# Optimization experiments

Hardware: AMD Instinct MI355X
Metric: run time of the kernel (lower is better)

The kernel has to match this reference:

```python
import jax, jax.numpy as jnp
import numpy as np

TAU = 0.1
LAMBD = 0.75
EPS = 1e-8  # torch cosine_similarity norm clamp


def setup_inputs() -> dict:
    key = jax.random.key(0)
    k1, k2 = jax.random.split(key)
    B, D = 8192, 768
    v = jax.random.normal(k1, (B, D), dtype=jnp.float32)
    u = jax.random.normal(k2, (B, D), dtype=jnp.float32)
    return {"v": v, "u": u}


def reference(v, u):
    # Batched equivalent of the per-sample Python loop:
    # cos(v_i, u_j) = <v_i/||v_i||, u_j/||u_j||>, with torch's eps clamp on norms.
    v = v.astype(jnp.float32)
    u = u.astype(jnp.float32)
    vn = v / jnp.maximum(jnp.linalg.norm(v, axis=1, keepdims=True), EPS)
    un = u / jnp.maximum(jnp.linalg.norm(u, axis=1, keepdims=True), EPS)
    sim = jnp.einsum('id,jd->ij', vn, un) / TAU  # [B, B] logits
    diag = jnp.diagonal(sim)
    # image->text: -log( exp(sim_ii) / sum_j exp(sim_ij) )
    loss_it = jax.nn.logsumexp(sim, axis=1) - diag
    # text->image: -log( exp(sim_ii) / sum_j exp(sim_ji) )
    loss_ti = jax.nn.logsumexp(sim, axis=0) - diag
    # In the torch source text_image calls .item(), detaching it from autograd.
    loss_ti = jax.lax.stop_gradient(loss_ti)
    return jnp.mean(LAMBD * loss_it + (1.0 - LAMBD) * loss_ti)
```

## Files before the change

### kernel.cpp

```cpp
#include <hip/hip_runtime.h>
#include <hip/hip_bf16.h>

typedef unsigned char u8;
typedef unsigned short u16;
typedef unsigned int u32;
typedef float f32x16 __attribute__((ext_vector_type(16)));
typedef float f32x2 __attribute__((ext_vector_type(2)));
typedef int i32x4 __attribute__((ext_vector_type(4)));
typedef int i32x8 __attribute__((ext_vector_type(8)));

#define B_SZ 8192
#define D_SZ 768
#define TAU_INV 10.0f
#define ESCALE 0.014088818758681283f
#define FP4_SCALE 32.0f
#define SCHRAU_K1 118185.58f
#define SCHRAU_K2 1064879685.0f


__device__ __forceinline__ u32 fp4_enc(float x) {
    float y = fabsf(x);
    u32 n = (u32)(y >= 0.25f) + (u32)(y >= 0.75f) + (u32)(y >= 1.25f) +
            (u32)(y >= 1.75f) + (u32)(y >= 2.5f)  + (u32)(y >= 3.5f) +
            (u32)(y >= 5.0f);
    return n | (x < 0.f ? 8u : 0u);
}

__device__ __forceinline__ u16 fp4_pack4(float x, float y, float z, float w) {
    return (u16)(fp4_enc(x) | (fp4_enc(y) << 4) | (fp4_enc(z) << 8) | (fp4_enc(w) << 12));
}

__global__ __launch_bounds__(256) void norm_kernel(const float4* __restrict__ v,
                                                   const float4* __restrict__ u,
                                                   u16* __restrict__ vn,
                                                   u16* __restrict__ un,
                                                   float* __restrict__ diag) {
    const int wid = threadIdx.x >> 6, lane = threadIdx.x & 63;
    const int row = blockIdx.x * 4 + wid;
    const float4* vr = v + (size_t)row * 192;
    const float4* ur = u + (size_t)row * 192;
    float4 a[3], b[3];
    float sv = 0.f, su = 0.f, sd = 0.f;
#pragma unroll
    for (int c = 0; c < 3; ++c) {
        a[c] = vr[lane + 64 * c];
        b[c] = ur[lane + 64 * c];
        sv += a[c].x * a[c].x + a[c].y * a[c].y + a[c].z * a[c].z + a[c].w * a[c].w;
        su += b[c].x * b[c].x + b[c].y * b[c].y + b[c].z * b[c].z + b[c].w * b[c].w;
        sd += a[c].x * b[c].x + a[c].y * b[c].y + a[c].z * b[c].z + a[c].w * b[c].w;
    }
#pragma unroll
    for (int m = 1; m < 64; m <<= 1) {
        sv += __shfl_xor(sv, m);
        su += __shfl_xor(su, m);
        sd += __shfl_xor(sd, m);
    }
    const float iv = FP4_SCALE / fmaxf(sqrtf(sv), 1e-8f);
    const float iu = FP4_SCALE / fmaxf(sqrtf(su), 1e-8f);
    const int rg = row >> 5, rr = row & 31;
#pragma unroll
    for (int c = 0; c < 3; ++c) {
        u16 pa = fp4_pack4(a[c].x * iv, a[c].y * iv, a[c].z * iv, a[c].w * iv);
        u16 pb = fp4_pack4(b[c].x * iu, b[c].y * iu, b[c].z * iu, b[c].w * iu);
        const int e = lane + 64 * c;
        const int idx = (rg * 12 + (e >> 4)) * 512 + ((e >> 3) & 1) * 256 + rr * 8 + (e & 7);
        vn[idx] = pa;
        un[idx] = pb;
    }
    if (lane == 0) diag[row] = sd * iv * iu * TAU_INV / (FP4_SCALE * FP4_SCALE);
}

__device__ __forceinline__ i32x8 ldsfrag(const u8* p) {
    i32x4 lo = *(const i32x4*)p;
    return __builtin_shufflevector(lo, lo, 0, 1, 2, 3, -1, -1, -1, -1);
}

__device__ __forceinline__ void gload_lds16(const u8* g, u8* l) {
    __builtin_amdgcn_global_load_lds((const __attribute__((address_space(1))) void*)g,
                                     (__attribute__((address_space(3))) void*)l, 16, 0, 0);
}

__device__ __forceinline__ f32x16 mx_mfma4(i32x8 a, i32x8 b, f32x16 c) {
    return __builtin_amdgcn_mfma_scale_f32_32x32x64_f8f6f4(
        a, b, c, 4, 4, 0, 0x7F7F7F7F, 0, 0x7F7F7F7F);
}

__global__ __launch_bounds__(1024, 4) void simexp_kernel(const u8* __restrict__ vn,
                                                         const u8* __restrict__ un,
                                                         float* __restrict__ rowP,
                                                         float* __restrict__ colP) {
    __shared__ __attribute__((aligned(16))) u8 stg[3][16][1024];
    __shared__ float rowLds[4][256];
    __shared__ float colLds[4][256];

    const int tid  = threadIdx.x;
    const int w    = tid >> 6;
    const int lane = tid & 63;
    const int l32  = lane & 31;
    const int h    = lane >> 5;
    const int wr = w >> 2, wc = w & 3;

    const int id = blockIdx.x;
    const int chunk = id >> 6;
    const int li = id & 63;
    const int rb = ((chunk >> 2) << 3) + (li >> 3);
    const int cb = ((chunk & 3) << 3) + (li & 7);

    const u8* gsrc = (w < 8 ? vn + (size_t)(rb * 8 + w) * 12288
                            : un + (size_t)(cb * 8 + (w - 8)) * 12288)
                     + (u32)lane * 16;

    f32x16 acc[2][2];
#pragma unroll
    for (int i = 0; i < 2; ++i)
#pragma unroll
        for (int j = 0; j < 2; ++j)
#pragma unroll
            for (int r = 0; r < 16; ++r) acc[i][j][r] = 0.f;

#define STAGE(t) gload_lds16(gsrc + (t) * 1024, &stg[(t) % 3][w][0]);

    STAGE(0)
    STAGE(1)
    asm volatile("s_waitcnt vmcnt(1)\n\ts_barrier" ::: "memory");

#pragma unroll
    for (int t = 0; t < 12; ++t) {
        if (t + 2 < 12) STAGE(t + 2)
        const u8* base = &stg[t % 3][0][0] + (u32)lane * 16;
        i32x8 fa0 = ldsfrag(base + (wr * 2)     * 1024);
        i32x8 fa1 = ldsfrag(base + (wr * 2 + 1) * 1024);
        i32x8 fb0 = ldsfrag(base + (8 + wc * 2) * 1024);
        i32x8 fb1 = ldsfrag(base + (9 + wc * 2) * 1024);
        __builtin_amdgcn_s_setprio(1);
        acc[0][0] = mx_mfma4(fa0, fb0, acc[0][0]);
        acc[1][0] = mx_mfma4(fa1, fb0, acc[1][0]);
        acc[0][1] = mx_mfma4(fa0, fb1, acc[0][1]);
        acc[1][1] = mx_mfma4(fa1, fb1, acc[1][1]);
        __builtin_amdgcn_s_setprio(0);
        if (t < 10)       asm volatile("s_waitcnt vmcnt(1)\n\ts_barrier" ::: "memory");
        else if (t == 10) asm volatile("s_waitcnt vmcnt(0)\n\ts_barrier" ::: "memory");
    }
#undef STAGE

    f32x2 val2[16];
    f32x2 cacc2[2];
#pragma unroll
    for (int p = 0; p < 16; ++p) { val2[p].x = 0.f; val2[p].y = 0.f; }
    cacc2[0].x = 0.f; cacc2[0].y = 0.f;
    cacc2[1].x = 0.f; cacc2[1].y = 0.f;
#pragma unroll
    for (int i = 0; i < 2; ++i)
#pragma unroll
        for (int j = 0; j < 2; ++j)
#pragma unroll
            for (int r = 0; r < 16; r += 2) {
                f32x2 a;
                a.x = acc[i][j][r];
                a.y = acc[i][j][r + 1];
                f32x2 t = a * SCHRAU_K1 + SCHRAU_K2;
                f32x2 e;
                e.x = __int_as_float((int)t.x);
                e.y = __int_as_float((int)t.y);
                val2[i * 8 + (r >> 1)] += e;
                cacc2[j] += e;
            }

#pragma unroll
    for (int m = 16; m >= 2; m >>= 1) {
        const int n = m >> 1;
        const bool hi = (l32 & m) != 0;
#pragma unroll
        for (int p = 0; p < n; ++p) {
            f32x2 a = val2[p], b = val2[p + n];
            f32x2 x, y;
            x.x = hi ? b.x : a.x;  x.y = hi ? b.y : a.y;
            y.x = hi ? a.x : b.x;  y.y = hi ? a.y : b.y;
            f32x2 s;
            s.x = __shfl_xor(y.x, m);
            s.y = __shfl_xor(y.y, m);
            val2[p] = x + s;
        }
    }
    {
        f32x2 s;
        s.x = __shfl_xor(val2[0].x, 1);
        s.y = __shfl_xor(val2[0].y, 1);
        val2[0] += s;
    }
    {
        const int q = (l32 >> 1) & 15;
        const int t = 2 * q + (l32 & 1);
        const int i = t >> 4, r = t & 15;
        const int row = wr * 64 + i * 32 + (r & 3) + 8 * (r >> 2) + 4 * h;
        rowLds[wc][row] = (l32 & 1) ? val2[0].y : val2[0].x;
    }
    {
        float c0 = cacc2[0].x + cacc2[0].y;
        float c1 = cacc2[1].x + cacc2[1].y;
        c0 += __shfl_xor(c0, 32);
        c1 += __shfl_xor(c1, 32);
        if (h == 0) {
            colLds[wr][wc * 64 + l32]      = c0;
            colLds[wr][wc * 64 + 32 + l32] = c1;
        }
    }
    __syncthreads();
    if (tid < 256) {
        rowP[(size_t)cb * B_SZ + rb * 256 + tid] =
            rowLds[0][tid] + rowLds[1][tid] + rowLds[2][tid] + rowLds[3][tid];
    } else if (tid < 512) {
        const int t = tid - 256;
        colP[(size_t)rb * B_SZ + cb * 256 + t] =
            colLds[0][t] + colLds[1][t] + colLds[2][t] + colLds[3][t];
    }
}

__global__ __launch_bounds__(256) void finalize_kernel(const float* __restrict__ rowP,
                                                       const float* __restrict__ colP,
                                                       const float* __restrict__ diag,
                                                       float* __restrict__ out) {
    const int i = blockIdx.x * 256 + threadIdx.x;
    float rs = 0.f, cs = 0.f;
#pragma unroll 8
    for (int p = 0; p < 32; ++p) {
        rs += rowP[(size_t)p * B_SZ + i];
        cs += colP[(size_t)p * B_SZ + i];
    }
    float contrib = (0.75f * logf(rs) + 0.25f * logf(cs) - diag[i]) * (1.0f / (float)B_SZ);
#pragma unroll
    for (int m = 1; m < 64; m <<= 1) contrib += __shfl_xor(contrib, m);
    __shared__ float red[4];
    const int wid = threadIdx.x >> 6, lane = threadIdx.x & 63;
    if (lane == 0) red[wid] = contrib;
    __syncthreads();
    if (threadIdx.x == 0) atomicAdd(out, red[0] + red[1] + red[2] + red[3]);
}

extern "C" void kernel_launch(void* const* d_in, const int* in_sizes, int n_in,
                              void* d_out, int out_size, void* d_ws, size_t ws_size,
                              hipStream_t stream) {
    const float* v = (const float*)d_in[0];
    const float* u = (const float*)d_in[1];
    char* ws = (char*)d_ws;
    u16* vn4   = (u16*)(ws);
    u16* un4   = (u16*)(ws + 3145728);
    float* dg  = (float*)(ws + 6291456);
    float* rwp = (float*)(ws + 6324224);
    float* clp = (float*)(ws + 7372800);
    float* out = (float*)d_out;

    hipMemsetAsync(out, 0, sizeof(float), stream);
    hipLaunchKernelGGL(norm_kernel, dim3(2048), dim3(256), 0, stream,
                       (const float4*)v, (const float4*)u, vn4, un4, dg);
    hipLaunchKernelGGL(simexp_kernel, dim3(1024), dim3(1024), 0, stream,
                       (const u8*)vn4, (const u8*)un4, rwp, clp);
    hipLaunchKernelGGL(finalize_kernel, dim3(B_SZ / 256), dim3(256), 0, stream, rwp, clp, dg, out);
}
```

Measured before the change: 125.5 us.

## Use 8-wave blocks with 128x64 per-wave tiles and double-K staging

Cuts the similarity/exp kernel from 16 waves to 8 waves per 256x256 block. Each wave now computes a 128x64 tile with 8 accumulators instead of 64x64 with 4, and each stage loads two K-chunks. This is meant to raise MFMA work per LDS fragment load, halve the number of barriers, and reduce cross-wave reductions. The cost is higher register pressure and fewer waves available to hide latency.

```diff
diff --git a/kernel.cpp b/kernel.cpp
--- a/kernel.cpp
+++ b/kernel.cpp
@@ -85,13 +85,13 @@
         a, b, c, 4, 4, 0, 0x7F7F7F7F, 0, 0x7F7F7F7F);
 }
 
-__global__ __launch_bounds__(1024, 4) void simexp_kernel(const u8* __restrict__ vn,
-                                                         const u8* __restrict__ un,
-                                                         float* __restrict__ rowP,
-                                                         float* __restrict__ colP) {
-    __shared__ __attribute__((aligned(16))) u8 stg[3][16][1024];
+__global__ __launch_bounds__(512, 2) void simexp_kernel(const u8* __restrict__ vn,
+                                                        const u8* __restrict__ un,
+                                                        float* __restrict__ rowP,
+                                                        float* __restrict__ colP) {
+    __shared__ __attribute__((aligned(16))) u8 stg[3][16][2][1024];
     __shared__ float rowLds[4][256];
-    __shared__ float colLds[4][256];
+    __shared__ float colLds[2][256];
 
     const int tid  = threadIdx.x;
     const int w    = tid >> 6;
@@ -106,51 +106,68 @@
     const int rb = ((chunk >> 2) << 3) + (li >> 3);
     const int cb = ((chunk & 3) << 3) + (li & 7);
 
-    const u8* gsrc = (w < 8 ? vn + (size_t)(rb * 8 + w) * 12288
-                            : un + (size_t)(cb * 8 + (w - 8)) * 12288)
-                     + (u32)lane * 16;
-
-    f32x16 acc[2][2];
-#pragma unroll
-    for (int i = 0; i < 2; ++i)
+    const u8* gA = vn + (size_t)(rb * 8 + w) * 12288 + (u32)lane * 16;
+    const u8* gB = un + (size_t)(cb * 8 + w) * 12288 + (u32)lane * 16;
+
+    f32x16 acc[4][2];
+#pragma unroll
+    for (int i = 0; i < 4; ++i)
 #pragma unroll
         for (int j = 0; j < 2; ++j)
 #pragma unroll
             for (int r = 0; r < 16; ++r) acc[i][j][r] = 0.f;
 
-#define STAGE(t) gload_lds16(gsrc + (t) * 1024, &stg[(t) % 3][w][0]);
+#define STAGE(t)                                                  \
+    {                                                             \
+        gload_lds16(gA + (2 * (t)) * 1024,     &stg[(t) % 3][w][0][0]);     \
+        gload_lds16(gA + (2 * (t) + 1) * 1024, &stg[(t) % 3][w][1][0]);     \
+        gload_lds16(gB + (2 * (t)) * 1024,     &stg[(t) % 3][8 + w][0][0]); \
+        gload_lds16(gB + (2 * (t) + 1) * 1024, &stg[(t) % 3][8 + w][1][0]); \
+    }
 
     STAGE(0)
     STAGE(1)
-    asm volatile("s_waitcnt vmcnt(1)\n\ts_barrier" ::: "memory");
-
-#pragma unroll
-    for (int t = 0; t < 12; ++t) {
-        if (t + 2 < 12) STAGE(t + 2)
-        const u8* base = &stg[t % 3][0][0] + (u32)lane * 16;
-        i32x8 fa0 = ldsfrag(base + (wr * 2)     * 1024);
-        i32x8 fa1 = ldsfrag(base + (wr * 2 + 1) * 1024);
-        i32x8 fb0 = ldsfrag(base + (8 + wc * 2) * 1024);
-        i32x8 fb1 = ldsfrag(base + (9 + wc * 2) * 1024);
-        __builtin_amdgcn_s_setprio(1);
-        acc[0][0] = mx_mfma4(fa0, fb0, acc[0][0]);
-        acc[1][0] = mx_mfma4(fa1, fb0, acc[1][0]);
-        acc[0][1] = mx_mfma4(fa0, fb1, acc[0][1]);
-        acc[1][1] = mx_mfma4(fa1, fb1, acc[1][1]);
-        __builtin_amdgcn_s_setprio(0);
-        if (t < 10)       asm volatile("s_waitcnt vmcnt(1)\n\ts_barrier" ::: "memory");
-        else if (t == 10) asm volatile("s_waitcnt vmcnt(0)\n\ts_barrier" ::: "memory");
+    asm volatile("s_waitcnt vmcnt(4)\n\ts_barrier" ::: "memory");
+
+#pragma unroll
+    for (int t = 0; t < 6; ++t) {
+        if (t + 2 < 6) STAGE(t + 2)
+        const u8* s = &stg[t % 3][0][0][0] + (u32)lane * 16;
+#pragma unroll
+        for (int kk = 0; kk < 2; ++kk) {
+            i32x8 fa0 = ldsfrag(s + ((wr * 4 + 0) * 2 + kk) * 1024);
+            i32x8 fa1 = ldsfrag(s + ((wr * 4 + 1) * 2 + kk) * 1024);
+            i32x8 fa2 = ldsfrag(s + ((wr * 4 + 2) * 2 + kk) * 1024);
+            i32x8 fa3 = ldsfrag(s + ((wr * 4 + 3) * 2 + kk) * 1024);
+            i32x8 fb0 = ldsfrag(s + ((8 + wc * 2 + 0) * 2 + kk) * 1024);
+            i32x8 fb1 = ldsfrag(s + ((8 + wc * 2 + 1) * 2 + kk) * 1024);
+            __builtin_amdgcn_s_setprio(1);
+            acc[0][0] = mx_mfma4(fa0, fb0, acc[0][0]);
+            acc[1][0] = mx_mfma4(fa1, fb0, acc[1][0]);
+            acc[2][0] = mx_mfma4(fa2, fb0, acc[2][0]);
+            acc[3][0] = mx_mfma4(fa3, fb0, acc[3][0]);
+            acc[0][1] = mx_mfma4(fa0, fb1, acc[0][1]);
+            acc[1][1] = mx_mfma4(fa1, fb1, acc[1][1]);
+            acc[2][1] = mx_mfma4(fa2, fb1, acc[2][1]);
+            acc[3][1] = mx_mfma4(fa3, fb1, acc[3][1]);
+            __builtin_amdgcn_s_setprio(0);
+        }
+        if (t < 4)       asm volatile("s_waitcnt vmcnt(4)\n\ts_barrier" ::: "memory");
+        else if (t == 4) asm volatile("s_waitcnt vmcnt(0)\n\ts_barrier" ::: "memory");
     }
 #undef STAGE
 
-    f32x2 val2[16];
+    f32x2 va[16], vb[16];
     f32x2 cacc2[2];
 #pragma unroll
-    for (int p = 0; p < 16; ++p) { val2[p].x = 0.f; val2[p].y = 0.f; }
+    for (int p = 0; p < 16; ++p) {
+        va[p].x = 0.f; va[p].y = 0.f;
+        vb[p].x = 0.f; vb[p].y = 0.f;
+    }
     cacc2[0].x = 0.f; cacc2[0].y = 0.f;
     cacc2[1].x = 0.f; cacc2[1].y = 0.f;
 #pragma unroll
-    for (int i = 0; i < 2; ++i)
+    for (int i = 0; i < 4; ++i)
 #pragma unroll
         for (int j = 0; j < 2; ++j)
 #pragma unroll
@@ -162,7 +179,8 @@
                 f32x2 e;
                 e.x = __int_as_float((int)t.x);
                 e.y = __int_as_float((int)t.y);
-                val2[i * 8 + (r >> 1)] += e;
+                if (i < 2) va[(i & 1) * 8 + (r >> 1)] += e;
+                else       vb[(i & 1) * 8 + (r >> 1)] += e;
                 cacc2[j] += e;
             }
 
@@ -172,28 +190,44 @@
         const bool hi = (l32 & m) != 0;
 #pragma unroll
         for (int p = 0; p < n; ++p) {
-            f32x2 a = val2[p], b = val2[p + n];
-            f32x2 x, y;
-            x.x = hi ? b.x : a.x;  x.y = hi ? b.y : a.y;
-            y.x = hi ? a.x : b.x;  y.y = hi ? a.y : b.y;
-            f32x2 s;
-            s.x = __shfl_xor(y.x, m);
-            s.y = __shfl_xor(y.y, m);
-            val2[p] = x + s;
+            {
+                f32x2 a = va[p], b = va[p + n];
+                f32x2 x, y;
+                x.x = hi ? b.x : a.x;  x.y = hi ? b.y : a.y;
+                y.x = hi ? a.x : b.x;  y.y = hi ? a.y : b.y;
+                f32x2 s;
+                s.x = __shfl_xor(y.x, m);
+                s.y = __shfl_xor(y.y, m);
+                va[p] = x + s;
+            }
+            {
+                f32x2 a = vb[p], b = vb[p + n];
+                f32x2 x, y;
+                x.x = hi ? b.x : a.x;  x.y = hi ? b.y : a.y;
+                y.x = hi ? a.x : b.x;  y.y = hi ? a.y : b.y;
+                f32x2 s;
+                s.x = __shfl_xor(y.x, m);
+                s.y = __shfl_xor(y.y, m);
+                vb[p] = x + s;
+            }
         }
     }
     {
         f32x2 s;
-        s.x = __shfl_xor(val2[0].x, 1);
-        s.y = __shfl_xor(val2[0].y, 1);
-        val2[0] += s;
+        s.x = __shfl_xor(va[0].x, 1);
+        s.y = __shfl_xor(va[0].y, 1);
+        va[0] += s;
+        s.x = __shfl_xor(vb[0].x, 1);
+        s.y = __shfl_xor(vb[0].y, 1);
+        vb[0] += s;
     }
     {
         const int q = (l32 >> 1) & 15;
-        const int t = 2 * q + (l32 & 1);
-        const int i = t >> 4, r = t & 15;
-        const int row = wr * 64 + i * 32 + (r & 3) + 8 * (r >> 2) + 4 * h;
-        rowLds[wc][row] = (l32 & 1) ? val2[0].y : val2[0].x;
+        const int tt = 2 * q + (l32 & 1);
+        const int i2 = tt >> 4, r2 = tt & 15;
+        const int rbase = i2 * 32 + (r2 & 3) + 8 * (r2 >> 2) + 4 * h;
+        rowLds[wc][wr * 128 + rbase]      = (l32 & 1) ? va[0].y : va[0].x;
+        rowLds[wc][wr * 128 + 64 + rbase] = (l32 & 1) ? vb[0].y : vb[0].x;
     }
     {
         float c0 = cacc2[0].x + cacc2[0].y;
@@ -209,10 +243,9 @@
     if (tid < 256) {
         rowP[(size_t)cb * B_SZ + rb * 256 + tid] =
             rowLds[0][tid] + rowLds[1][tid] + rowLds[2][tid] + rowLds[3][tid];
-    } else if (tid < 512) {
+    } else {
         const int t = tid - 256;
-        colP[(size_t)rb * B_SZ + cb * 256 + t] =
-            colLds[0][t] + colLds[1][t] + colLds[2][t] + colLds[3][t];
+        colP[(size_t)rb * B_SZ + cb * 256 + t] = colLds[0][t] + colLds[1][t];
     }
 }
 
@@ -253,7 +286,7 @@
     hipMemsetAsync(out, 0, sizeof(float), stream);
     hipLaunchKernelGGL(norm_kernel, dim3(2048), dim3(256), 0, stream,
                        (const float4*)v, (const float4*)u, vn4, un4, dg);
-    hipLaunchKernelGGL(simexp_kernel, dim3(1024), dim3(1024), 0, stream,
+    hipLaunchKernelGGL(simexp_kernel, dim3(1024), dim3(512), 0, stream,
                        (const u8*)vn4, (const u8*)un4, rwp, clp);
     hipLaunchKernelGGL(finalize_kernel, dim3(B_SZ / 256), dim3(256), 0, stream, rwp, clp, dg, out);
 }
```

Measured after the change: 129.2 us. +3.0%, slower.

## Retile similarity kernel to 256x128 tiles with 512-thread blocks and deeper k-steps

Applied to the files above, without the earlier changes.

Blocks go from 1024 threads computing 256x256 tiles to 512 threads (8 waves) computing 256x128 tiles. Each pipeline stage now loads 2 KB k-slices, so there are 6 stages of two MFMA k-steps each, and every wave issues three LDS-direct loads per stage. Block IDs are remapped for L2 locality, and the reduction scratch reuses the staging LDS. The finalize kernel now sums 64 row partials instead of 32. Smaller blocks may schedule more flexibly, but the smaller column tile costs reuse of the v operand and doubles the row-partial traffic.

```diff
diff --git a/kernel.cpp b/kernel.cpp
--- a/kernel.cpp
+++ b/kernel.cpp
@@ -85,30 +85,39 @@
         a, b, c, 4, 4, 0, 0x7F7F7F7F, 0, 0x7F7F7F7F);
 }
 
-__global__ __launch_bounds__(1024, 4) void simexp_kernel(const u8* __restrict__ vn,
-                                                         const u8* __restrict__ un,
-                                                         float* __restrict__ rowP,
-                                                         float* __restrict__ colP) {
-    __shared__ __attribute__((aligned(16))) u8 stg[3][16][1024];
-    __shared__ float rowLds[4][256];
-    __shared__ float colLds[4][256];
+__global__ __launch_bounds__(512, 4) void simexp_kernel(const u8* __restrict__ vn,
+                                                        const u8* __restrict__ un,
+                                                        float* __restrict__ rowP,
+                                                        float* __restrict__ colP) {
+    __shared__ __attribute__((aligned(16))) u8 stg[3][24][1024];
 
     const int tid  = threadIdx.x;
     const int w    = tid >> 6;
     const int lane = tid & 63;
     const int l32  = lane & 31;
     const int h    = lane >> 5;
-    const int wr = w >> 2, wc = w & 3;
-
-    const int id = blockIdx.x;
+    const int wr = w >> 1, wc = w & 1;
+
+    const int id0 = blockIdx.x;
+    const int id  = (id0 & 7) * 256 + (id0 >> 3);
     const int chunk = id >> 6;
     const int li = id & 63;
-    const int rb = ((chunk >> 2) << 3) + (li >> 3);
-    const int cb = ((chunk & 3) << 3) + (li & 7);
-
-    const u8* gsrc = (w < 8 ? vn + (size_t)(rb * 8 + w) * 12288
-                            : un + (size_t)(cb * 8 + (w - 8)) * 12288)
-                     + (u32)lane * 16;
+    const int rb = (chunk >> 3) * 8 + (li >> 3);
+    const int cb = (chunk & 7) * 8 + (li & 7);
+
+    const u8* gt[3];
+#pragma unroll
+    for (int q = 0; q < 3; ++q) {
+        const int T = 3 * w + q;
+        const u8* p;
+        if (T < 16) {
+            p = vn + (size_t)(rb * 8 + (T >> 1)) * 12288 + (size_t)(T & 1) * 1024;
+        } else {
+            const int S = T - 16;
+            p = un + (size_t)(cb * 4 + (S >> 1)) * 12288 + (size_t)(S & 1) * 1024;
+        }
+        gt[q] = p + (u32)lane * 16;
+    }
 
     f32x16 acc[2][2];
 #pragma unroll
@@ -118,30 +127,41 @@
 #pragma unroll
             for (int r = 0; r < 16; ++r) acc[i][j][r] = 0.f;
 
-#define STAGE(t) gload_lds16(gsrc + (t) * 1024, &stg[(t) % 3][w][0]);
+#define STAGE(t)                                                        \
+    {                                                                   \
+        gload_lds16(gt[0] + (t) * 2048, &stg[(t) % 3][3 * w + 0][0]);   \
+        gload_lds16(gt[1] + (t) * 2048, &stg[(t) % 3][3 * w + 1][0]);   \
+        gload_lds16(gt[2] + (t) * 2048, &stg[(t) % 3][3 * w + 2][0]);   \
+    }
 
     STAGE(0)
     STAGE(1)
-    asm volatile("s_waitcnt vmcnt(1)\n\ts_barrier" ::: "memory");
-
-#pragma unroll
-    for (int t = 0; t < 12; ++t) {
-        if (t + 2 < 12) STAGE(t + 2)
-        const u8* base = &stg[t % 3][0][0] + (u32)lane * 16;
-        i32x8 fa0 = ldsfrag(base + (wr * 2)     * 1024);
-        i32x8 fa1 = ldsfrag(base + (wr * 2 + 1) * 1024);
-        i32x8 fb0 = ldsfrag(base + (8 + wc * 2) * 1024);
-        i32x8 fb1 = ldsfrag(base + (9 + wc * 2) * 1024);
-        __builtin_amdgcn_s_setprio(1);
-        acc[0][0] = mx_mfma4(fa0, fb0, acc[0][0]);
-        acc[1][0] = mx_mfma4(fa1, fb0, acc[1][0]);
-        acc[0][1] = mx_mfma4(fa0, fb1, acc[0][1]);
-        acc[1][1] = mx_mfma4(fa1, fb1, acc[1][1]);
-        __builtin_amdgcn_s_setprio(0);
-        if (t < 10)       asm volatile("s_waitcnt vmcnt(1)\n\ts_barrier" ::: "memory");
-        else if (t == 10) asm volatile("s_waitcnt vmcnt(0)\n\ts_barrier" ::: "memory");
+    asm volatile("s_waitcnt vmcnt(3)\n\ts_barrier" ::: "memory");
+
+#pragma unroll
+    for (int t = 0; t < 6; ++t) {
+        if (t + 2 < 6) STAGE(t + 2)
+        const u8* s = &stg[t % 3][0][0] + (u32)lane * 16;
+#pragma unroll
+        for (int kk = 0; kk < 2; ++kk) {
+            i32x8 fa0 = ldsfrag(s + (((wr * 2 + 0) * 2 + kk)) * 1024);
+            i32x8 fa1 = ldsfrag(s + (((wr * 2 + 1) * 2 + kk)) * 1024);
+            i32x8 fb0 = ldsfrag(s + ((16 + (wc * 2 + 0) * 2 + kk)) * 1024);
+            i32x8 fb1 = ldsfrag(s + ((16 + (wc * 2 + 1) * 2 + kk)) * 1024);
+            __builtin_amdgcn_s_setprio(1);
+            acc[0][0] = mx_mfma4(fa0, fb0, acc[0][0]);
+            acc[1][0] = mx_mfma4(fa1, fb0, acc[1][0]);
+            acc[0][1] = mx_mfma4(fa0, fb1, acc[0][1]);
+            acc[1][1] = mx_mfma4(fa1, fb1, acc[1][1]);
+            __builtin_amdgcn_s_setprio(0);
+        }
+        if (t < 4)       asm volatile("s_waitcnt vmcnt(3)\n\ts_barrier" ::: "memory");
+        else if (t == 4) asm volatile("s_waitcnt vmcnt(0)\n\ts_barrier" ::: "memory");
     }
 #undef STAGE
+
+    float* rowRed = (float*)&stg[0][0][0];
+    float* colRed = rowRed + 512;
 
     f32x2 val2[16];
     f32x2 cacc2[2];
@@ -190,10 +210,10 @@
     }
     {
         const int q = (l32 >> 1) & 15;
-        const int t = 2 * q + (l32 & 1);
-        const int i = t >> 4, r = t & 15;
-        const int row = wr * 64 + i * 32 + (r & 3) + 8 * (r >> 2) + 4 * h;
-        rowLds[wc][row] = (l32 & 1) ? val2[0].y : val2[0].x;
+        const int tt = 2 * q + (l32 & 1);
+        const int i2 = tt >> 4, r2 = tt & 15;
+        const int rbase = i2 * 32 + (r2 & 3) + 8 * (r2 >> 2) + 4 * h;
+        rowRed[wc * 256 + wr * 64 + rbase] = (l32 & 1) ? val2[0].y : val2[0].x;
     }
     {
         float c0 = cacc2[0].x + cacc2[0].y;
@@ -201,18 +221,17 @@
         c0 += __shfl_xor(c0, 32);
         c1 += __shfl_xor(c1, 32);
         if (h == 0) {
-            colLds[wr][wc * 64 + l32]      = c0;
-            colLds[wr][wc * 64 + 32 + l32] = c1;
+            colRed[wr * 128 + wc * 64 + l32]      = c0;
+            colRed[wr * 128 + wc * 64 + 32 + l32] = c1;
         }
     }
     __syncthreads();
     if (tid < 256) {
-        rowP[(size_t)cb * B_SZ + rb * 256 + tid] =
-            rowLds[0][tid] + rowLds[1][tid] + rowLds[2][tid] + rowLds[3][tid];
-    } else if (tid < 512) {
+        rowP[(size_t)cb * B_SZ + rb * 256 + tid] = rowRed[tid] + rowRed[256 + tid];
+    } else if (tid < 384) {
         const int t = tid - 256;
-        colP[(size_t)rb * B_SZ + cb * 256 + t] =
-            colLds[0][t] + colLds[1][t] + colLds[2][t] + colLds[3][t];
+        colP[(size_t)rb * B_SZ + cb * 128 + t] =
+            colRed[t] + colRed[128 + t] + colRed[256 + t] + colRed[384 + t];
     }
 }
 
@@ -223,10 +242,9 @@
     const int i = blockIdx.x * 256 + threadIdx.x;
     float rs = 0.f, cs = 0.f;
 #pragma unroll 8
-    for (int p = 0; p < 32; ++p) {
-        rs += rowP[(size_t)p * B_SZ + i];
-        cs += colP[(size_t)p * B_SZ + i];
-    }
+    for (int p = 0; p < 64; ++p) rs += rowP[(size_t)p * B_SZ + i];
+#pragma unroll 8
+    for (int p = 0; p < 32; ++p) cs += colP[(size_t)p * B_SZ + i];
     float contrib = (0.75f * logf(rs) + 0.25f * logf(cs) - diag[i]) * (1.0f / (float)B_SZ);
 #pragma unroll
     for (int m = 1; m < 64; m <<= 1) contrib += __shfl_xor(contrib, m);
@@ -247,13 +265,13 @@
     u16* un4   = (u16*)(ws + 3145728);
     float* dg  = (float*)(ws + 6291456);
     float* rwp = (float*)(ws + 6324224);
-    float* clp = (float*)(ws + 7372800);
+    float* clp = (float*)(ws + 8421376);
     float* out = (float*)d_out;
 
     hipMemsetAsync(out, 0, sizeof(float), stream);
     hipLaunchKernelGGL(norm_kernel, dim3(2048), dim3(256), 0, stream,
                        (const float4*)v, (const float4*)u, vn4, un4, dg);
-    hipLaunchKernelGGL(simexp_kernel, dim3(1024), dim3(1024), 0, stream,
+    hipLaunchKernelGGL(simexp_kernel, dim3(2048), dim3(512), 0, stream,
                        (const u8*)vn4, (const u8*)un4, rwp, clp);
     hipLaunchKernelGGL(finalize_kernel, dim3(B_SZ / 256), dim3(256), 0, stream, rwp, clp, dg, out);
 }
```

Measured after the change: 128.2 us. +2.2%, slower.
